# Kernel optimization log

Measured on AMD Instinct MI355X. Metric: run time of the kernel, lower is better.

The kernel has to match this reference:

```python
import jax, jax.numpy as jnp
import numpy as np

N_NODES = 100000


def gcn_conv(x, W, b, src, dst, n):
    h = x @ W  # transform first (PyG GCNConv order), smaller edge traffic
    loops = jnp.arange(n, dtype=src.dtype)
    s = jnp.concatenate([src, loops])
    d = jnp.concatenate([dst, loops])
    deg = jax.ops.segment_sum(jnp.ones_like(d, dtype=h.dtype), d, num_segments=n)
    dinv = jnp.where(deg > 0, jax.lax.rsqrt(deg), 0.0)
    norm = dinv[s] * dinv[d]  # [E+N]
    msg = h[s] * norm[:, None]  # gather + scale
    out = jax.ops.segment_sum(msg, d, num_segments=n)  # scatter-add
    return out + b


def setup_inputs() -> dict:
    key = jax.random.key(0)
    ks = jax.random.split(key, 8)
    x = jax.random.normal(ks[0], (N_NODES, 256), dtype=jnp.float32)
    edge_index = jax.random.randint(ks[1], (2, 1600000), 0, N_NODES, dtype=jnp.int64)
    pos_edge_index = jax.random.randint(ks[2], (2, 200000), 0, N_NODES, dtype=jnp.int64)
    neg_edge_index = jax.random.randint(ks[3], (2, 200000), 0, N_NODES, dtype=jnp.int64)
    W1 = jax.random.normal(ks[4], (256, 128), dtype=jnp.float32) * (1.0 / np.sqrt(256))
    b1 = jnp.zeros((128,), dtype=jnp.float32)
    W2 = jax.random.normal(ks[5], (128, 8), dtype=jnp.float32) * (1.0 / np.sqrt(128))
    b2 = jnp.zeros((8,), dtype=jnp.float32)
    return {"x": x, "edge_index": edge_index, "pos_edge_index": pos_edge_index,
            "neg_edge_index": neg_edge_index, "W1": W1, "b1": b1, "W2": W2, "b2": b2}


def reference(x, edge_index, pos_edge_index, neg_edge_index, W1, b1, W2, b2):
    n = x.shape[0]
    src, dst = edge_index[0], edge_index[1]
    h = jax.nn.relu(gcn_conv(x, W1, b1, src, dst, n))
    z = gcn_conv(h, W2, b2, src, dst, n)  # [N, 8]
    ei = jnp.concatenate([pos_edge_index, neg_edge_index], axis=-1)
    return jnp.sum(z[ei[0]] * z[ei[1]], axis=-1)  # [E_pos + E_neg]
```

## Files before the change

kernel.cpp:

```cpp
#include <hip/hip_runtime.h>

constexpr int N   = 100000;
constexpr int E   = 1600000;
constexpr int EP  = 200000;
constexpr int ES  = 400000;
constexpr int CAP = 64;
constexpr int XG2 = 128;
constexpr int DR2 = (N + XG2 - 1) / XG2;
constexpr int SEGCAP = 14336;
constexpr int EPB = 8192;
constexpr int PBS = 1024;
constexpr int NPB = (E + EPB - 1) / EPB;
constexpr int BSTR = 264;

typedef _Float16 f16x8 __attribute__((ext_vector_type(8)));
typedef _Float16 f16x4 __attribute__((ext_vector_type(4)));
typedef _Float16 f16x2 __attribute__((ext_vector_type(2)));
typedef float    f32x4 __attribute__((ext_vector_type(4)));

__global__ __launch_bounds__(1024) void partition_edges(const int* __restrict__ ei,
                                                        int* __restrict__ gcnt,
                                                        unsigned* __restrict__ eb) {
    __shared__ int lh[XG2];
    __shared__ int rk[XG2];
    const int tid = threadIdx.x;
    const int e0  = blockIdx.x * EPB;
    if (tid < XG2) lh[tid] = 0;
    __syncthreads();
#pragma unroll
    for (int i = 0; i < EPB; i += PBS) {
        const int e = e0 + i + tid;
        if (e < E) {
            const int d = ei[E + e];
            atomicAdd(&lh[d / DR2], 1);
        }
    }
    __syncthreads();
    if (tid < XG2) rk[tid] = atomicAdd(&gcnt[tid], lh[tid]);
    __syncthreads();
#pragma unroll
    for (int i = 0; i < EPB; i += PBS) {
        const int e = e0 + i + tid;
        if (e < E) {
            const int s   = ei[e];
            const int d   = ei[E + e];
            const int g   = d / DR2;
            const int rel = d - g * DR2;
            const int p   = atomicAdd(&rk[g], 1);
            if (p < SEGCAP)
                eb[(size_t)g * SEGCAP + p] = ((unsigned)rel << 17) | (unsigned)s;
        }
    }
}

__global__ __launch_bounds__(1024) void fill_csr(const unsigned* __restrict__ eb,
                                                 const int* __restrict__ gcnt,
                                                 int* __restrict__ cnt,
                                                 int* __restrict__ rp,
                                                 float* __restrict__ dinv,
                                                 int* __restrict__ colc) {
    __shared__ int hcnt[1024];
    __shared__ int wsum[16];
    __shared__ unsigned stage[SEGCAP];
    const int g   = blockIdx.x;
    const int tid = threadIdx.x;
    const int cg  = min(gcnt[g], SEGCAP);
    const unsigned* seg = eb + (size_t)g * SEGCAP;

    hcnt[tid] = 0;
    __syncthreads();
    for (int i = tid; i < cg; i += 1024)
        atomicAdd(&hcnt[seg[i] >> 17], 1);
    __syncthreads();

    const int c    = hcnt[tid];
    const int lane = tid & 63;
    const int wid  = tid >> 6;
    int incl = c;
#pragma unroll
    for (int off = 1; off < 64; off <<= 1) {
        const int v = __shfl_up(incl, off);
        if (lane >= off) incl += v;
    }
    if (lane == 63) wsum[wid] = incl;
    __syncthreads();
    if (tid < 16) {
        int v = wsum[tid];
#pragma unroll
        for (int off = 1; off < 16; off <<= 1) {
            const int u = __shfl_up(v, off);
            if (tid >= off) v += u;
        }
        wsum[tid] = v;
    }
    __syncthreads();
    const int excl = incl - c + (wid ? wsum[wid - 1] : 0);

    const int base = g * DR2;
    if (tid < DR2 && base + tid < N) {
        cnt [base + tid] = c;
        rp  [base + tid] = g * SEGCAP + excl;
        dinv[base + tid] = rsqrtf((float)c + 1.0f);
    }
    __syncthreads();
    hcnt[tid] = excl;
    __syncthreads();

    for (int i = tid; i < cg; i += 1024) {
        const unsigned pk = seg[i];
        const int p = atomicAdd(&hcnt[pk >> 17], 1);
        stage[p] = pk & 0x1FFFFu;
    }
    __syncthreads();
    for (int i = tid; i < cg; i += 1024)
        colc[(size_t)g * SEGCAP + i] = (int)stage[i];
}

__global__ __launch_bounds__(256) void w1_transpose(const float* __restrict__ W1,
                                                    _Float16* __restrict__ W1T) {
    const int n = blockIdx.x;
    const int k = threadIdx.x;
    W1T[n * 256 + k] = (_Float16)W1[(size_t)k * 128 + n];
}

__global__ __launch_bounds__(256) void gemm1_mfma(const float* __restrict__ X,
                                                  const _Float16* __restrict__ W1T,
                                                  _Float16* __restrict__ H) {
    __shared__ _Float16 Bs[128][BSTR];

    const int tid  = threadIdx.x;
    const int wave = tid >> 6;
    const int lane = tid & 63;
    const int m16  = lane & 15;
    const int quad = lane >> 4;
    const int rowBase = blockIdx.x * 256 + wave * 64;

#pragma unroll
    for (int i = 0; i < 16; ++i) {
        const int c  = tid + 256 * i;
        const int n  = c >> 5;
        const int kb = (c & 31) * 16;
        *(f16x8*)((char*)&Bs[n][0] + kb) = *(const f16x8*)((const char*)W1T + (size_t)c * 16);
    }
    __syncthreads();

    f32x4 acc[4][8] = {};
    f32x4 avA[8];

    auto loadA = [&](int k0) {
#pragma unroll
        for (int m = 0; m < 4; ++m) {
            int gr = rowBase + m * 16 + m16;
            gr = gr < N ? gr : N - 1;
            const f32x4* p = (const f32x4*)&X[(size_t)gr * 256 + k0 + quad * 8];
            avA[2 * m]     = __builtin_nontemporal_load(p);
            avA[2 * m + 1] = __builtin_nontemporal_load(p + 1);
        }
    };

    loadA(0);
    for (int k0 = 0; k0 < 256; k0 += 32) {
        f16x8 af[4];
#pragma unroll
        for (int m = 0; m < 4; ++m) {
            f16x8 h;
            h[0] = (_Float16)avA[2*m][0];   h[1] = (_Float16)avA[2*m][1];
            h[2] = (_Float16)avA[2*m][2];   h[3] = (_Float16)avA[2*m][3];
            h[4] = (_Float16)avA[2*m+1][0]; h[5] = (_Float16)avA[2*m+1][1];
            h[6] = (_Float16)avA[2*m+1][2]; h[7] = (_Float16)avA[2*m+1][3];
            af[m] = h;
        }
        if (k0 + 32 < 256) loadA(k0 + 32);
#pragma unroll
        for (int nt = 0; nt < 8; ++nt) {
            const f16x8 bf = *(const f16x8*)&Bs[nt * 16 + m16][k0 + quad * 8];
#pragma unroll
            for (int m = 0; m < 4; ++m)
                acc[m][nt] = __builtin_amdgcn_mfma_f32_16x16x32_f16(af[m], bf, acc[m][nt], 0, 0, 0);
        }
    }

#pragma unroll
    for (int m = 0; m < 4; ++m)
#pragma unroll
        for (int nt = 0; nt < 8; ++nt)
#pragma unroll
            for (int r = 0; r < 4; ++r) {
                const int gm = rowBase + m * 16 + quad * 4 + r;
                if (gm < N) H[(size_t)gm * 128 + nt * 16 + m16] = (_Float16)acc[m][nt][r];
            }
}

__global__ __launch_bounds__(256) void agg1_gemm2(const _Float16* __restrict__ H,
                                                  const int* __restrict__ cnt,
                                                  const int* __restrict__ rp,
                                                  const int* __restrict__ colc,
                                                  const float* __restrict__ dinv,
                                                  const float* __restrict__ b1,
                                                  const float* __restrict__ W2,
                                                  float* __restrict__ Z) {
    const int nw   = (blockIdx.x * blockDim.x + threadIdx.x) >> 6;
    const int lane = threadIdx.x & 63;
    if (nw >= N) return;
    const int n   = __builtin_amdgcn_readfirstlane(nw);
    const int c   = min(__builtin_amdgcn_readfirstlane(cnt[n]), CAP);
    const int rpn = __builtin_amdgcn_readfirstlane(rp[n]);
    const float dn = dinv[n];

    const _Float16* hbase = H + lane * 2;

    const float2 b   = *(const float2*)&b1[lane * 2];
    const float4 wa0 = *(const float4*)&W2[(size_t)(lane * 2) * 8];
    const float4 wa1 = *(const float4*)&W2[(size_t)(lane * 2) * 8 + 4];
    const float4 wb0 = *(const float4*)&W2[(size_t)(lane * 2 + 1) * 8];
    const float4 wb1 = *(const float4*)&W2[(size_t)(lane * 2 + 1) * 8 + 4];

    f16x2 va[8]; float wa[8];
#pragma unroll
    for (int t = 0; t < 8; ++t) {
        const int ec = t < c ? t : c;
        const int s  = (ec < c) ? colc[rpn + ec] : n;
        wa[t] = (t <= c) ? dinv[s] : 0.f;
        va[t] = *(const f16x2*)&hbase[(size_t)s * 128];
    }
    float ax = 0.f, ay = 0.f;
    const int tot8 = (c + 1 + 7) & ~7;
    for (int j = 8; j < tot8; j += 8) {
        f16x2 vb[8]; float wb[8];
#pragma unroll
        for (int t = 0; t < 8; ++t) {
            const int e  = j + t;
            const int ec = e < c ? e : c;
            const int s  = (ec < c) ? colc[rpn + ec] : n;
            wb[t] = (e <= c) ? dinv[s] : 0.f;
            vb[t] = *(const f16x2*)&hbase[(size_t)s * 128];
        }
#pragma unroll
        for (int t = 0; t < 8; ++t) {
            ax = fmaf(wa[t], (float)va[t][0], ax);
            ay = fmaf(wa[t], (float)va[t][1], ay);
            va[t] = vb[t]; wa[t] = wb[t];
        }
    }
#pragma unroll
    for (int t = 0; t < 8; ++t) {
        ax = fmaf(wa[t], (float)va[t][0], ax);
        ay = fmaf(wa[t], (float)va[t][1], ay);
    }

    const float hr0 = fmaxf(ax * dn + b.x, 0.f);
    const float hr1 = fmaxf(ay * dn + b.y, 0.f);

    float p[8];
    p[0] = hr0 * wa0.x + hr1 * wb0.x;
    p[1] = hr0 * wa0.y + hr1 * wb0.y;
    p[2] = hr0 * wa0.z + hr1 * wb0.z;
    p[3] = hr0 * wa0.w + hr1 * wb0.w;
    p[4] = hr0 * wa1.x + hr1 * wb1.x;
    p[5] = hr0 * wa1.y + hr1 * wb1.y;
    p[6] = hr0 * wa1.z + hr1 * wb1.z;
    p[7] = hr0 * wa1.w + hr1 * wb1.w;
#pragma unroll
    for (int off = 32; off > 0; off >>= 1)
#pragma unroll
        for (int j = 0; j < 8; ++j) p[j] += __shfl_xor(p[j], off);
    if (lane == 0) {
        *(float4*)&Z[(size_t)n * 8]     = make_float4(p[0], p[1], p[2], p[3]);
        *(float4*)&Z[(size_t)n * 8 + 4] = make_float4(p[4], p[5], p[6], p[7]);
    }
}

__global__ __launch_bounds__(256) void agg2(const float* __restrict__ Z,
                                            const int* __restrict__ cnt,
                                            const int* __restrict__ rp,
                                            const int* __restrict__ colc,
                                            const float* __restrict__ dinv,
                                            const float* __restrict__ b2,
                                            float* __restrict__ ZA) {
    const int t = blockIdx.x * blockDim.x + threadIdx.x;
    const int n = t >> 3;
    const int f = t & 7;
    if (n >= N) return;
    const int c   = min(cnt[n], CAP);
    const int rpn = rp[n];

    float acc = 0.f;
    float zv[4], wv[4];
#pragma unroll
    for (int tt = 0; tt < 4; ++tt) {
        const int s = (tt < c) ? colc[rpn + tt] : n;
        wv[tt] = (tt < c) ? dinv[s] : 0.0f;
        zv[tt] = Z[(size_t)s * 8 + f];
    }
    for (int j = 4; j + 4 <= c + 4; j += 4) {
        float zb[4], wb[4];
#pragma unroll
        for (int tt = 0; tt < 4; ++tt) {
            const int jt = j + tt;
            const int s  = (jt < c) ? colc[rpn + jt] : n;
            wb[tt] = (jt < c) ? dinv[s] : 0.0f;
            zb[tt] = Z[(size_t)s * 8 + f];
        }
#pragma unroll
        for (int tt = 0; tt < 4; ++tt) {
            acc = fmaf(wv[tt], zv[tt], acc);
            zv[tt] = zb[tt]; wv[tt] = wb[tt];
        }
    }
#pragma unroll
    for (int tt = 0; tt < 4; ++tt) acc = fmaf(wv[tt], zv[tt], acc);

    const float dn = dinv[n];
    const float zn = Z[(size_t)n * 8 + f];
    ZA[(size_t)n * 8 + f] = (acc + dn * zn) * dn + b2[f];
}

__global__ __launch_bounds__(256) void score(const float* __restrict__ ZA,
                                             const int* __restrict__ pe,
                                             const int* __restrict__ ne,
                                             float* __restrict__ out) {
    const int e = blockIdx.x * blockDim.x + threadIdx.x;
    if (e >= ES) return;
    int a, b;
    if (e < EP) { a = pe[e];      b = pe[EP + e]; }
    else        { a = ne[e - EP]; b = ne[e];      }
    const float4 xa0 = *(const float4*)&ZA[(size_t)a * 8];
    const float4 xa1 = *(const float4*)&ZA[(size_t)a * 8 + 4];
    const float4 xb0 = *(const float4*)&ZA[(size_t)b * 8];
    const float4 xb1 = *(const float4*)&ZA[(size_t)b * 8 + 4];
    out[e] = xa0.x * xb0.x + xa0.y * xb0.y + xa0.z * xb0.z + xa0.w * xb0.w +
             xa1.x * xb1.x + xa1.y * xb1.y + xa1.z * xb1.z + xa1.w * xb1.w;
}


extern "C" void kernel_launch(void* const* d_in, const int* in_sizes, int n_in,
                              void* d_out, int out_size, void* d_ws, size_t ws_size,
                              hipStream_t stream) {
    const float* x  = (const float*)d_in[0];
    const int*   ei = (const int*)d_in[1];
    const int*   pe = (const int*)d_in[2];
    const int*   ne = (const int*)d_in[3];
    const float* W1 = (const float*)d_in[4];
    const float* b1 = (const float*)d_in[5];
    const float* W2 = (const float*)d_in[6];
    const float* b2 = (const float*)d_in[7];
    float* out = (float*)d_out;

    char* ws = (char*)d_ws;
    size_t off = 0;
    auto carve = [&](size_t bytes) {
        char* p = ws + off;
        off += (bytes + 255) & ~(size_t)255;
        return p;
    };
    int*       gcnt = (int*)      carve((size_t)XG2 * sizeof(int));
    int*       cnt  = (int*)      carve((size_t)N * sizeof(int));
    int*       rp   = (int*)      carve((size_t)N * sizeof(int));
    float*     dinv = (float*)    carve((size_t)N * sizeof(float));
    unsigned*  eb   = (unsigned*) carve((size_t)XG2 * SEGCAP * sizeof(unsigned));
    int*       colc = (int*)      carve((size_t)XG2 * SEGCAP * sizeof(int));
    _Float16*  H    = (_Float16*) carve((size_t)N * 128 * sizeof(_Float16));
    float*     Z    = (float*)    carve((size_t)N * 8 * sizeof(float));
    float*     ZA   = (float*)    carve((size_t)N * 8 * sizeof(float));
    _Float16*  W1T  = (_Float16*) carve((size_t)128 * 256 * sizeof(_Float16));

    hipMemsetAsync(gcnt, 0, (size_t)XG2 * sizeof(int), stream);
    partition_edges<<<NPB, PBS, 0, stream>>>(ei, gcnt, eb);
    w1_transpose   <<<128, 256, 0, stream>>>(W1, W1T);
    fill_csr       <<<XG2, 1024, 0, stream>>>(eb, gcnt, cnt, rp, dinv, colc);
    gemm1_mfma     <<<(N + 255) / 256, 256, 0, stream>>>(x, W1T, H);
    agg1_gemm2     <<<((size_t)N * 64 + 255) / 256, 256, 0, stream>>>(H, cnt, rp, colc, dinv, b1, W2, Z);
    agg2           <<<((size_t)N * 8 + 255) / 256, 256, 0, stream>>>(Z, cnt, rp, colc, dinv, b2, ZA);
    score          <<<(ES + 255) / 256, 256, 0, stream>>>(ZA, pe, ne, out);
}
```

Before: 348.7 us.

## Split layer-1 aggregation into feature slabs with pre-scaled H and separate GEMM2

GEMM1 now multiplies each output row by dinv of its source node and writes H into eight 16-feature slabs ([8][N][16]). This removes the per-edge dinv gather from the aggregation. A new agg1s kernel handles one slab per block, with four edge groups per wave reducing via shuffles, so each slab (about 3.2MB) can stay cache-resident during the random gathers. The fused agg1+GEMM2 kernel is split: ReLU outputs go to an fp32 Hr buffer and a separate gemm2k kernel computes Z, which adds an extra launch and roughly 51MB of extra write and read traffic.

After: 505.6 us. 1.45x slower.

```diff
diff --git a/kernel.cpp b/kernel.cpp
--- a/kernel.cpp
+++ b/kernel.cpp
@@ -125,7 +125,8 @@
 
 __global__ __launch_bounds__(256) void gemm1_mfma(const float* __restrict__ X,
                                                   const _Float16* __restrict__ W1T,
-                                                  _Float16* __restrict__ H) {
+                                                  const float* __restrict__ dinv,
+                                                  _Float16* __restrict__ Hs) {
     __shared__ _Float16 Bs[128][BSTR];
 
     const int tid  = threadIdx.x;
@@ -180,6 +181,14 @@
         }
     }
 
+    float dv[4][4];
+#pragma unroll
+    for (int m = 0; m < 4; ++m)
+#pragma unroll
+        for (int r = 0; r < 4; ++r) {
+            const int gm = rowBase + m * 16 + quad * 4 + r;
+            dv[m][r] = (gm < N) ? dinv[gm] : 0.f;
+        }
 #pragma unroll
     for (int m = 0; m < 4; ++m)
 #pragma unroll
@@ -187,79 +196,94 @@
 #pragma unroll
             for (int r = 0; r < 4; ++r) {
                 const int gm = rowBase + m * 16 + quad * 4 + r;
-                if (gm < N) H[(size_t)gm * 128 + nt * 16 + m16] = (_Float16)acc[m][nt][r];
+                if (gm < N)
+                    Hs[(size_t)nt * N * 16 + (size_t)gm * 16 + m16] =
+                        (_Float16)(acc[m][nt][r] * dv[m][r]);
             }
 }
 
-__global__ __launch_bounds__(256) void agg1_gemm2(const _Float16* __restrict__ H,
-                                                  const int* __restrict__ cnt,
-                                                  const int* __restrict__ rp,
-                                                  const int* __restrict__ colc,
-                                                  const float* __restrict__ dinv,
-                                                  const float* __restrict__ b1,
-                                                  const float* __restrict__ W2,
-                                                  float* __restrict__ Z) {
+__global__ __launch_bounds__(512) void agg1s(const _Float16* __restrict__ Hs,
+                                             const int* __restrict__ cnt,
+                                             const int* __restrict__ rp,
+                                             const int* __restrict__ colc,
+                                             const float* __restrict__ dinv,
+                                             const float* __restrict__ b1,
+                                             float* __restrict__ Hr) {
+    const int k  = blockIdx.x & 7;
+    const int nw = (blockIdx.x >> 3) * 8 + (threadIdx.x >> 6);
+    if (nw >= N) return;
+    const int lane = threadIdx.x & 63;
+    const int eg   = lane >> 4;
+    const int f    = lane & 15;
+    const int n    = __builtin_amdgcn_readfirstlane(nw);
+    const int c    = min(__builtin_amdgcn_readfirstlane(cnt[n]), CAP);
+    const int rpn  = __builtin_amdgcn_readfirstlane(rp[n]);
+
+    const _Float16* hb = Hs + (size_t)k * N * 16 + f;
+
+    float a = 0.f;
+    const int tot4 = (c + 1 + 3) & ~3;
+    int s0[4]; float m0[4]; _Float16 v0[4];
+#pragma unroll
+    for (int t = 0; t < 4; ++t) {
+        const int e   = eg + 4 * t;
+        const int ecl = e < c ? e : (c > 0 ? c - 1 : 0);
+        s0[t] = (e < c) ? colc[rpn + ecl] : n;
+        m0[t] = (e <= c) ? 1.f : 0.f;
+    }
+#pragma unroll
+    for (int t = 0; t < 4; ++t) v0[t] = hb[(size_t)s0[t] * 16];
+    for (int j = 16; j < tot4; j += 16) {
+        int s1[4]; float m1[4]; _Float16 v1[4];
+#pragma unroll
+        for (int t = 0; t < 4; ++t) {
+            const int e   = eg + j + 4 * t;
+            const int ecl = e < c ? e : (c > 0 ? c - 1 : 0);
+            s1[t] = (e < c) ? colc[rpn + ecl] : n;
+            m1[t] = (e <= c) ? 1.f : 0.f;
+        }
+#pragma unroll
+        for (int t = 0; t < 4; ++t) v1[t] = hb[(size_t)s1[t] * 16];
+#pragma unroll
+        for (int t = 0; t < 4; ++t) {
+            a = fmaf(m0[t], (float)v0[t], a);
+            v0[t] = v1[t]; m0[t] = m1[t];
+        }
+    }
+#pragma unroll
+    for (int t = 0; t < 4; ++t) a = fmaf(m0[t], (float)v0[t], a);
+
+    a += __shfl_xor(a, 16);
+    a += __shfl_xor(a, 32);
+
+    const float h = fmaxf(fmaf(a, dinv[n], b1[k * 16 + f]), 0.f);
+    if (eg == 0) Hr[((size_t)k * N + n) * 16 + f] = h;
+}
+
+__global__ __launch_bounds__(256) void gemm2k(const float* __restrict__ Hr,
+                                              const float* __restrict__ W2,
+                                              float* __restrict__ Z) {
     const int nw   = (blockIdx.x * blockDim.x + threadIdx.x) >> 6;
     const int lane = threadIdx.x & 63;
     if (nw >= N) return;
-    const int n   = __builtin_amdgcn_readfirstlane(nw);
-    const int c   = min(__builtin_amdgcn_readfirstlane(cnt[n]), CAP);
-    const int rpn = __builtin_amdgcn_readfirstlane(rp[n]);
-    const float dn = dinv[n];
-
-    const _Float16* hbase = H + lane * 2;
-
-    const float2 b   = *(const float2*)&b1[lane * 2];
-    const float4 wa0 = *(const float4*)&W2[(size_t)(lane * 2) * 8];
-    const float4 wa1 = *(const float4*)&W2[(size_t)(lane * 2) * 8 + 4];
-    const float4 wb0 = *(const float4*)&W2[(size_t)(lane * 2 + 1) * 8];
-    const float4 wb1 = *(const float4*)&W2[(size_t)(lane * 2 + 1) * 8 + 4];
-
-    f16x2 va[8]; float wa[8];
-#pragma unroll
-    for (int t = 0; t < 8; ++t) {
-        const int ec = t < c ? t : c;
-        const int s  = (ec < c) ? colc[rpn + ec] : n;
-        wa[t] = (t <= c) ? dinv[s] : 0.f;
-        va[t] = *(const f16x2*)&hbase[(size_t)s * 128];
-    }
-    float ax = 0.f, ay = 0.f;
-    const int tot8 = (c + 1 + 7) & ~7;
-    for (int j = 8; j < tot8; j += 8) {
-        f16x2 vb[8]; float wb[8];
-#pragma unroll
-        for (int t = 0; t < 8; ++t) {
-            const int e  = j + t;
-            const int ec = e < c ? e : c;
-            const int s  = (ec < c) ? colc[rpn + ec] : n;
-            wb[t] = (e <= c) ? dinv[s] : 0.f;
-            vb[t] = *(const f16x2*)&hbase[(size_t)s * 128];
-        }
-#pragma unroll
-        for (int t = 0; t < 8; ++t) {
-            ax = fmaf(wa[t], (float)va[t][0], ax);
-            ay = fmaf(wa[t], (float)va[t][1], ay);
-            va[t] = vb[t]; wa[t] = wb[t];
-        }
-    }
-#pragma unroll
-    for (int t = 0; t < 8; ++t) {
-        ax = fmaf(wa[t], (float)va[t][0], ax);
-        ay = fmaf(wa[t], (float)va[t][1], ay);
-    }
-
-    const float hr0 = fmaxf(ax * dn + b.x, 0.f);
-    const float hr1 = fmaxf(ay * dn + b.y, 0.f);
-
+    const int n  = __builtin_amdgcn_readfirstlane(nw);
+    const int k  = lane >> 3;
+    const int f2 = (lane & 7) * 2;
+    const float2 h2 = *(const float2*)&Hr[((size_t)k * N + n) * 16 + f2];
+    const int row = k * 16 + f2;
+    const float4 wa0 = *(const float4*)&W2[(size_t)row * 8];
+    const float4 wa1 = *(const float4*)&W2[(size_t)row * 8 + 4];
+    const float4 wb0 = *(const float4*)&W2[(size_t)(row + 1) * 8];
+    const float4 wb1 = *(const float4*)&W2[(size_t)(row + 1) * 8 + 4];
     float p[8];
-    p[0] = hr0 * wa0.x + hr1 * wb0.x;
-    p[1] = hr0 * wa0.y + hr1 * wb0.y;
-    p[2] = hr0 * wa0.z + hr1 * wb0.z;
-    p[3] = hr0 * wa0.w + hr1 * wb0.w;
-    p[4] = hr0 * wa1.x + hr1 * wb1.x;
-    p[5] = hr0 * wa1.y + hr1 * wb1.y;
-    p[6] = hr0 * wa1.z + hr1 * wb1.z;
-    p[7] = hr0 * wa1.w + hr1 * wb1.w;
+    p[0] = h2.x * wa0.x + h2.y * wb0.x;
+    p[1] = h2.x * wa0.y + h2.y * wb0.y;
+    p[2] = h2.x * wa0.z + h2.y * wb0.z;
+    p[3] = h2.x * wa0.w + h2.y * wb0.w;
+    p[4] = h2.x * wa1.x + h2.y * wb1.x;
+    p[5] = h2.x * wa1.y + h2.y * wb1.y;
+    p[6] = h2.x * wa1.z + h2.y * wb1.z;
+    p[7] = h2.x * wa1.w + h2.y * wb1.w;
 #pragma unroll
     for (int off = 32; off > 0; off >>= 1)
 #pragma unroll
@@ -358,8 +382,9 @@
     int*       rp   = (int*)      carve((size_t)N * sizeof(int));
     float*     dinv = (float*)    carve((size_t)N * sizeof(float));
     unsigned*  eb   = (unsigned*) carve((size_t)XG2 * SEGCAP * sizeof(unsigned));
-    int*       colc = (int*)      carve((size_t)XG2 * SEGCAP * sizeof(int));
-    _Float16*  H    = (_Float16*) carve((size_t)N * 128 * sizeof(_Float16));
+    int*       colc = (int*)      carve(((size_t)XG2 * SEGCAP + 64) * sizeof(int));
+    _Float16*  Hs   = (_Float16*) carve((size_t)8 * N * 16 * sizeof(_Float16));
+    float*     Hr   = (float*)    carve((size_t)8 * N * 16 * sizeof(float));
     float*     Z    = (float*)    carve((size_t)N * 8 * sizeof(float));
     float*     ZA   = (float*)    carve((size_t)N * 8 * sizeof(float));
     _Float16*  W1T  = (_Float16*) carve((size_t)128 * 256 * sizeof(_Float16));
@@ -368,8 +393,9 @@
     partition_edges<<<NPB, PBS, 0, stream>>>(ei, gcnt, eb);
     w1_transpose   <<<128, 256, 0, stream>>>(W1, W1T);
     fill_csr       <<<XG2, 1024, 0, stream>>>(eb, gcnt, cnt, rp, dinv, colc);
-    gemm1_mfma     <<<(N + 255) / 256, 256, 0, stream>>>(x, W1T, H);
-    agg1_gemm2     <<<((size_t)N * 64 + 255) / 256, 256, 0, stream>>>(H, cnt, rp, colc, dinv, b1, W2, Z);
+    gemm1_mfma     <<<(N + 255) / 256, 256, 0, stream>>>(x, W1T, dinv, Hs);
+    agg1s          <<<8 * ((N + 7) / 8), 512, 0, stream>>>(Hs, cnt, rp, colc, dinv, b1, Hr);
+    gemm2k         <<<((size_t)N * 64 + 255) / 256, 256, 0, stream>>>(Hr, W2, Z);
     agg2           <<<((size_t)N * 8 + 255) / 256, 256, 0, stream>>>(Z, cnt, rp, colc, dinv, b2, ZA);
     score          <<<(ES + 255) / 256, 256, 0, stream>>>(ZA, pe, ne, out);
 }
```
